# Kernel tuning notes

Measured on AMD Instinct MI355X. Metric: run time of the kernel, lower is better.

## Reference

```python
import jax, jax.numpy as jnp
import numpy as np

B, T, D, H = 2, 2048, 1024, 16
DK = D // H


def setup_inputs() -> dict:
    key = jax.random.key(0)
    ks = jax.random.split(key, 5)
    scale = 1.0 / np.sqrt(D)  # keep activations sane (xavier-like)
    return {
        "x": jax.random.normal(ks[0], (B, T, D), dtype=jnp.float32),
        "mask": jnp.zeros((B, 1, 1, T), dtype=jnp.float32),
        "Wq": jax.random.normal(ks[1], (D, D), dtype=jnp.float32) * scale,
        "Wk": jax.random.normal(ks[2], (D, D), dtype=jnp.float32) * scale,
        "Wv": jax.random.normal(ks[3], (D, D), dtype=jnp.float32) * scale,
        "Wo": jax.random.normal(ks[4], (D, D), dtype=jnp.float32) * scale,
    }


def reference(x, mask, Wq, Wk, Wv, Wo):
    b, t, d = x.shape
    h = H
    dk = d // h
    inv_sqrt_dk = jnp.asarray(1.0 / np.sqrt(dk), dtype=x.dtype)
    q = (x @ Wq).reshape(b, t, h, dk) * inv_sqrt_dk  # [b,t,h,dk]
    k = (x @ Wk).reshape(b, t, h, dk)
    v = (x @ Wv).reshape(b, t, h, dk)
    scores = jnp.einsum('bthd,blhd->bhtl', q, k) + mask  # [b,h,t,l]
    A = jax.nn.softmax(scores, axis=-1)
    # NOTE: faithful to the source: values are indexed by t (query pos), not l.
    o = jnp.einsum('bhtl,bthd->bhtd', A, v)  # [b,h,t,dk]
    # Faithful to source's raw reshape of (b,h,t,dk) -> (b,T,d)
    o = o.reshape(b, t, d)
    # nn.Linear without bias: y = o @ Wo^T
    return o @ Wo.T
```

## Files before the change

### kernel.cpp

```cpp
#include <hip/hip_runtime.h>
#include <hip/hip_bf16.h>


using bf16 = __hip_bfloat16;
typedef __attribute__((ext_vector_type(8))) short bf16x8;
typedef __attribute__((ext_vector_type(4))) float f32x4;

__device__ __forceinline__ void gld_lds16(const void* g, void* l) {
    __builtin_amdgcn_global_load_lds(
        (const __attribute__((address_space(1))) void*)g,
        (__attribute__((address_space(3))) void*)l, 16, 0, 0);
}

__global__ __launch_bounds__(256) void prep(const float* __restrict__ x,
                                            const float* __restrict__ Wv,
                                            const float* __restrict__ Wo,
                                            bf16* __restrict__ xb,
                                            bf16* __restrict__ WvT,
                                            bf16* __restrict__ Wob) {
    __shared__ float tile[64][65];
    const int id = blockIdx.x;
    const int t  = threadIdx.x;
    if (id < 256) {
        const int bx = id & 15, by = id >> 4;
        const int c = t & 63, r4 = t >> 6;
#pragma unroll
        for (int p = 0; p < 16; ++p) {
            int r = p * 4 + r4;
            tile[r][c] = Wv[(size_t)(by * 64 + r) * 1024 + bx * 64 + c];
        }
        __syncthreads();
#pragma unroll
        for (int p = 0; p < 16; ++p) {
            int r = p * 4 + r4;
            WvT[(size_t)(bx * 64 + r) * 1024 + by * 64 + c] = __float2bfloat16(tile[c][r]);
        }
    } else if (id < 4352) {
        const int i = (id - 256) * 256 + t;
        const float4 v = ((const float4*)x)[i];
        bf16 o[4] = {__float2bfloat16(v.x), __float2bfloat16(v.y),
                     __float2bfloat16(v.z), __float2bfloat16(v.w)};
        ((ulong1*)xb)[i] = *(ulong1*)o;
    } else {
        const int i = (id - 4352) * 256 + t;
        const float4 v = ((const float4*)Wo)[i];
        bf16 o[4] = {__float2bfloat16(v.x), __float2bfloat16(v.y),
                     __float2bfloat16(v.z), __float2bfloat16(v.w)};
        ((ulong1*)Wob)[i] = *(ulong1*)o;
    }
}

__device__ __forceinline__ void storeC(float v, bf16* p)  { *p = __float2bfloat16(v); }
__device__ __forceinline__ void storeC(float v, float* p) { *p = v; }

template <bool PERMUTE, typename OutT>
__global__ __launch_bounds__(256) void gemm_bt(const bf16* __restrict__ A,
                                               const bf16* __restrict__ Bt,
                                               OutT* __restrict__ C) {
    __shared__ __align__(16) bf16 st[2][6144];

    const int tid  = threadIdx.x;
    const int wave = tid >> 6;
    const int lane = tid & 63;
    const int m0 = blockIdx.x * 128;
    const int n0 = blockIdx.y * 64;

    const int wr = (wave >> 1) * 64;
    const int wc = (wave & 1) * 32;

    const int srow = tid >> 2;
    const int scol = (((tid & 3) ^ ((tid >> 3) & 3)) & 3) * 8;
    const bf16* gA = A  + (size_t)(m0 + srow) * 1024 + scol;
    const bf16* gB = Bt + (size_t)(n0 + srow) * 1024 + scol;
    const int woff = wave * 512;

    f32x4 acc[4][2];
#pragma unroll
    for (int i = 0; i < 4; ++i)
#pragma unroll
        for (int j = 0; j < 2; ++j)
            acc[i][j] = (f32x4){0.f, 0.f, 0.f, 0.f};

    const int fr = lane & 15;
    const int q8 = ((((lane >> 4) ^ (lane >> 1)) & 3)) * 8;

    {
        bf16* s = st[0];
        gld_lds16(gA,             s + woff);
        gld_lds16(gA + 64 * 1024, s + 2048 + woff);
        gld_lds16(gB,             s + 4096 + woff);
    }

    for (int i = 0; i < 32; ++i) {
        __syncthreads();
        if (i < 31) {
            const int kt = (i + 1) * 32;
            bf16* s = st[(i + 1) & 1];
            gld_lds16(gA + kt,             s + woff);
            gld_lds16(gA + kt + 64 * 1024, s + 2048 + woff);
            gld_lds16(gB + kt,             s + 4096 + woff);
        }

        const bf16* sAb = st[i & 1];
        const bf16* sBb = st[i & 1] + 4096;
        bf16x8 aF[4], bF[2];
#pragma unroll
        for (int ii = 0; ii < 4; ++ii)
            aF[ii] = *(const bf16x8*)&sAb[(wr + ii * 16 + fr) * 32 + q8];
#pragma unroll
        for (int j = 0; j < 2; ++j)
            bF[j] = *(const bf16x8*)&sBb[(wc + j * 16 + fr) * 32 + q8];
#pragma unroll
        for (int ii = 0; ii < 4; ++ii)
#pragma unroll
            for (int j = 0; j < 2; ++j)
                acc[ii][j] = __builtin_amdgcn_mfma_f32_16x16x32_bf16(
                    aF[ii], bF[j], acc[ii][j], 0, 0, 0);
    }

#pragma unroll
    for (int i = 0; i < 4; ++i) {
#pragma unroll
        for (int j = 0; j < 2; ++j) {
            const int col = n0 + wc + j * 16 + (lane & 15);
#pragma unroll
            for (int r = 0; r < 4; ++r) {
                const int row = m0 + wr + i * 16 + (lane >> 4) * 4 + r;
                if (PERMUTE) {
                    const int b = row >> 11, t = row & 2047;
                    const int h = col >> 6,  k = col & 63;
                    const int rr = (b << 11) | (h << 7) | (t >> 4);
                    const int cc = ((t & 15) << 6) | k;
                    storeC(acc[i][j][r], &C[(size_t)rr * 1024 + cc]);
                } else {
                    storeC(acc[i][j][r], &C[(size_t)row * 1024 + col]);
                }
            }
        }
    }
}

extern "C" void kernel_launch(void* const* d_in, const int* in_sizes, int n_in,
                              void* d_out, int out_size, void* d_ws, size_t ws_size,
                              hipStream_t stream) {
    (void)in_sizes; (void)n_in; (void)out_size; (void)ws_size;
    const float* x  = (const float*)d_in[0];
    const float* Wv = (const float*)d_in[4];
    const float* Wo = (const float*)d_in[5];
    float* out = (float*)d_out;

    bf16* xb    = (bf16*)d_ws;
    bf16* WvT   = xb    + 4096 * 1024;
    bf16* Wob   = WvT   + 1024 * 1024;
    bf16* vperm = Wob   + 1024 * 1024;

    prep<<<5376, 256, 0, stream>>>(x, Wv, Wo, xb, WvT, Wob);
    gemm_bt<true,  bf16 ><<<dim3(32, 16), 256, 0, stream>>>(xb, WvT, vperm);
    gemm_bt<false, float><<<dim3(32, 16), 256, 0, stream>>>(vperm, Wob, out);
}
```

Before: 115.7 us.

## Fuse prep and both GEMMs into one persistent kernel with grid barriers

Replaces the three launches (conversion/transpose prep plus two bf16 GEMMs) with one 512-block kernel. Each block first does its share of the conversion work, then runs the two GEMM phases, with atomic-counter grid barriers between phases. This removes launch overhead and inter-kernel gaps. It adds a memset of the barrier counters and depends on all 512 blocks being co-resident to avoid deadlock; launch_bounds(256,2) is set to help occupancy.

```diff
diff --git a/kernel.cpp b/kernel.cpp
--- a/kernel.cpp
+++ b/kernel.cpp
@@ -6,65 +6,39 @@
 typedef __attribute__((ext_vector_type(8))) short bf16x8;
 typedef __attribute__((ext_vector_type(4))) float f32x4;
 
+#define NBLK 512
+
 __device__ __forceinline__ void gld_lds16(const void* g, void* l) {
     __builtin_amdgcn_global_load_lds(
         (const __attribute__((address_space(1))) void*)g,
         (__attribute__((address_space(3))) void*)l, 16, 0, 0);
 }
 
-__global__ __launch_bounds__(256) void prep(const float* __restrict__ x,
-                                            const float* __restrict__ Wv,
-                                            const float* __restrict__ Wo,
-                                            bf16* __restrict__ xb,
-                                            bf16* __restrict__ WvT,
-                                            bf16* __restrict__ Wob) {
-    __shared__ float tile[64][65];
-    const int id = blockIdx.x;
-    const int t  = threadIdx.x;
-    if (id < 256) {
-        const int bx = id & 15, by = id >> 4;
-        const int c = t & 63, r4 = t >> 6;
-#pragma unroll
-        for (int p = 0; p < 16; ++p) {
-            int r = p * 4 + r4;
-            tile[r][c] = Wv[(size_t)(by * 64 + r) * 1024 + bx * 64 + c];
-        }
-        __syncthreads();
-#pragma unroll
-        for (int p = 0; p < 16; ++p) {
-            int r = p * 4 + r4;
-            WvT[(size_t)(bx * 64 + r) * 1024 + by * 64 + c] = __float2bfloat16(tile[c][r]);
-        }
-    } else if (id < 4352) {
-        const int i = (id - 256) * 256 + t;
-        const float4 v = ((const float4*)x)[i];
-        bf16 o[4] = {__float2bfloat16(v.x), __float2bfloat16(v.y),
-                     __float2bfloat16(v.z), __float2bfloat16(v.w)};
-        ((ulong1*)xb)[i] = *(ulong1*)o;
-    } else {
-        const int i = (id - 4352) * 256 + t;
-        const float4 v = ((const float4*)Wo)[i];
-        bf16 o[4] = {__float2bfloat16(v.x), __float2bfloat16(v.y),
-                     __float2bfloat16(v.z), __float2bfloat16(v.w)};
-        ((ulong1*)Wob)[i] = *(ulong1*)o;
+__device__ __forceinline__ void grid_barrier(int* cnt) {
+    __syncthreads();
+    __threadfence();
+    if (threadIdx.x == 0) {
+        __hip_atomic_fetch_add(cnt, 1, __ATOMIC_ACQ_REL, __HIP_MEMORY_SCOPE_AGENT);
+        while (__hip_atomic_load(cnt, __ATOMIC_ACQUIRE, __HIP_MEMORY_SCOPE_AGENT) < NBLK)
+            __builtin_amdgcn_s_sleep(2);
     }
+    __syncthreads();
+    __threadfence();
 }
 
 __device__ __forceinline__ void storeC(float v, bf16* p)  { *p = __float2bfloat16(v); }
 __device__ __forceinline__ void storeC(float v, float* p) { *p = v; }
 
 template <bool PERMUTE, typename OutT>
-__global__ __launch_bounds__(256) void gemm_bt(const bf16* __restrict__ A,
-                                               const bf16* __restrict__ Bt,
-                                               OutT* __restrict__ C) {
-    __shared__ __align__(16) bf16 st[2][6144];
-
-    const int tid  = threadIdx.x;
+__device__ __forceinline__ void gemm_body(const bf16* __restrict__ A,
+                                          const bf16* __restrict__ Bt,
+                                          OutT* __restrict__ C,
+                                          int bx, int by,
+                                          bf16 (*st)[6144], int tid) {
     const int wave = tid >> 6;
     const int lane = tid & 63;
-    const int m0 = blockIdx.x * 128;
-    const int n0 = blockIdx.y * 64;
-
+    const int m0 = bx * 128;
+    const int n0 = by * 64;
     const int wr = (wave >> 1) * 64;
     const int wc = (wave & 1) * 32;
 
@@ -100,7 +74,6 @@
             gld_lds16(gA + kt + 64 * 1024, s + 2048 + woff);
             gld_lds16(gB + kt,             s + 4096 + woff);
         }
-
         const bf16* sAb = st[i & 1];
         const bf16* sBb = st[i & 1] + 4096;
         bf16x8 aF[4], bF[2];
@@ -140,6 +113,59 @@
     }
 }
 
+__global__ __launch_bounds__(256, 2)
+void fused_mha(const float* __restrict__ x, const float* __restrict__ Wv,
+               const float* __restrict__ Wo,
+               bf16* __restrict__ xb, bf16* __restrict__ WvT,
+               bf16* __restrict__ Wob, bf16* __restrict__ vperm,
+               float* __restrict__ out, int* __restrict__ sync) {
+    __shared__ __align__(16) bf16 st[2][6144];
+    const int id  = blockIdx.x;
+    const int tid = threadIdx.x;
+
+#pragma unroll
+    for (int s = 0; s < 8; ++s) {
+        const int i = id * 2048 + s * 256 + tid;
+        const float4 v = ((const float4*)x)[i];
+        bf16 o[4] = {__float2bfloat16(v.x), __float2bfloat16(v.y),
+                     __float2bfloat16(v.z), __float2bfloat16(v.w)};
+        ((ulong1*)xb)[i] = *(ulong1*)o;
+    }
+    if (id < 256) {
+        float (*tile)[65] = (float(*)[65])st;
+        const int bx = id & 15, by = id >> 4;
+        const int c = tid & 63, r4 = tid >> 6;
+#pragma unroll
+        for (int p = 0; p < 16; ++p) {
+            int r = p * 4 + r4;
+            tile[r][c] = Wv[(size_t)(by * 64 + r) * 1024 + bx * 64 + c];
+        }
+        __syncthreads();
+#pragma unroll
+        for (int p = 0; p < 16; ++p) {
+            int r = p * 4 + r4;
+            WvT[(size_t)(bx * 64 + r) * 1024 + by * 64 + c] = __float2bfloat16(tile[c][r]);
+        }
+    } else {
+#pragma unroll
+        for (int s = 0; s < 4; ++s) {
+            const int i = (id - 256) * 1024 + s * 256 + tid;
+            const float4 v = ((const float4*)Wo)[i];
+            bf16 o[4] = {__float2bfloat16(v.x), __float2bfloat16(v.y),
+                         __float2bfloat16(v.z), __float2bfloat16(v.w)};
+            ((ulong1*)Wob)[i] = *(ulong1*)o;
+        }
+    }
+
+    grid_barrier(sync + 0);
+
+    gemm_body<true, bf16>(xb, WvT, vperm, id & 31, id >> 5, st, tid);
+
+    grid_barrier(sync + 16);
+
+    gemm_body<false, float>(vperm, Wob, out, id & 31, id >> 5, st, tid);
+}
+
 extern "C" void kernel_launch(void* const* d_in, const int* in_sizes, int n_in,
                               void* d_out, int out_size, void* d_ws, size_t ws_size,
                               hipStream_t stream) {
@@ -149,12 +175,12 @@
     const float* Wo = (const float*)d_in[5];
     float* out = (float*)d_out;
 
-    bf16* xb    = (bf16*)d_ws;
-    bf16* WvT   = xb    + 4096 * 1024;
-    bf16* Wob   = WvT   + 1024 * 1024;
-    bf16* vperm = Wob   + 1024 * 1024;
+    int*  sync  = (int*)d_ws;
+    bf16* xb    = (bf16*)((char*)d_ws + 256);
+    bf16* WvT   = xb  + 4096 * 1024;
+    bf16* Wob   = WvT + 1024 * 1024;
+    bf16* vperm = Wob + 1024 * 1024;
 
-    prep<<<5376, 256, 0, stream>>>(x, Wv, Wo, xb, WvT, Wob);
-    gemm_bt<true,  bf16 ><<<dim3(32, 16), 256, 0, stream>>>(xb, WvT, vperm);
-    gemm_bt<false, float><<<dim3(32, 16), 256, 0, stream>>>(vperm, Wob, out);
+    hipMemsetAsync(d_ws, 0, 256, stream);
+    fused_mha<<<NBLK, 256, 0, stream>>>(x, Wv, Wo, xb, WvT, Wob, vperm, out, sync);
 }
```

Measured after the change: 331.4 us. +186.4%, slower.
